# Performance work log

Hardware: AMD Instinct MI355X
Metric: run time of the kernel (lower is better)

## Reference

```python
import jax, jax.numpy as jnp
import numpy as np

B, S, H = 2, 1024, 2048          # batch, seq, hidden
E, K = 8, 2                       # num experts, top-k
I = 1408                          # moe_intermediate_size
IS = 5632                         # shared_expert_intermediate_size
WSCALE = 0.02


def setup_inputs() -> dict:
    key = jax.random.key(0)
    ks = jax.random.split(key, 9)
    f32 = jnp.float32
    return {
        "hidden_states": jax.random.normal(ks[0], (B, S, H), dtype=f32),
        "gate_w": jax.random.normal(ks[1], (E, H), dtype=f32) * WSCALE,          # router
        "w_gate": jax.random.normal(ks[2], (E, H, I), dtype=f32) * WSCALE,       # experts.N.gate_proj
        "w_up": jax.random.normal(ks[3], (E, H, I), dtype=f32) * WSCALE,         # experts.N.up_proj
        "w_down": jax.random.normal(ks[4], (E, I, H), dtype=f32) * WSCALE,       # experts.N.down_proj
        "sw_gate": jax.random.normal(ks[5], (H, IS), dtype=f32) * WSCALE,        # shared_expert.gate_proj
        "sw_up": jax.random.normal(ks[6], (H, IS), dtype=f32) * WSCALE,          # shared_expert.up_proj
        "sw_down": jax.random.normal(ks[7], (IS, H), dtype=f32) * WSCALE,        # shared_expert.down_proj
        "shared_gate_w": jax.random.normal(ks[8], (H, 1), dtype=f32) * WSCALE,   # shared_expert_gate
    }


def reference(hidden_states, gate_w, w_gate, w_up, w_down, sw_gate, sw_up, sw_down, shared_gate_w):
    x = hidden_states                                   # [B,S,H]
    # ---- TopKGate: softmax router -> top-k weights + indices, renormalized ----
    logits = jnp.einsum("bsh,eh->bse", x, gate_w)       # [B,S,E]
    probs = jax.nn.softmax(logits, axis=-1)
    top_w, top_i = jax.lax.top_k(probs, K)              # [B,S,K]
    top_w = top_w / jnp.sum(top_w, axis=-1, keepdims=True)
    # dense combine weights per expert: sum_k top_w * (top_i == e)  -> [B,S,E]
    onehot = jax.nn.one_hot(top_i, E, dtype=x.dtype)    # [B,S,K,E]
    combine = jnp.einsum("bsk,bske->bse", top_w, onehot)
    # ---- dense all-experts SwiGLU MLP, then mask/combine (faithful to source) ----
    g = jnp.einsum("bsh,ehi->besi", x, w_gate)          # [B,E,S,I]
    u = jnp.einsum("bsh,ehi->besi", x, w_up)
    h = jax.nn.silu(g) * u
    expert_out = jnp.einsum("besi,eih->besh", h, w_down)  # [B,E,S,H]
    moe_out = jnp.einsum("besh,bse->bsh", expert_out, combine)
    # ---- shared expert with sigmoid gate ----
    sh = jax.nn.silu(x @ sw_gate) * (x @ sw_up)         # [B,S,IS]
    shared_out = sh @ sw_down                            # [B,S,H]
    shared_gate = jax.nn.sigmoid(x @ shared_gate_w)     # [B,S,1]
    return moe_out + shared_out * shared_gate
```

## Files before the change

### kernel.cpp

```cpp
#include <hip/hip_runtime.h>
#include <hip/hip_bf16.h>
#include <stdint.h>

#define TOK   2048
#define HDIM  2048
#define IDIM  1408
#define ISDIM 5632
#define NEXP  8

typedef float  f32x4  __attribute__((ext_vector_type(4)));
typedef short  bf16x8 __attribute__((ext_vector_type(8)));

__device__ __forceinline__ unsigned short f2b(float f) {
  union { float f; uint32_t u; } v; v.f = f;
  return (unsigned short)((v.u + 0x7fffu + ((v.u >> 16) & 1u)) >> 16);
}

__device__ __forceinline__ void async16(void* lds, const void* g) {
  __builtin_amdgcn_global_load_lds(
      (const __attribute__((address_space(1))) unsigned int*)g,
      (__attribute__((address_space(3))) unsigned int*)lds, 16, 0, 0);
}

#define VWAIT_BAR(N) asm volatile("s_waitcnt vmcnt(" #N ")\n\ts_barrier" ::: "memory")
#define VBAR()       asm volatile("s_barrier" ::: "memory")

__global__ __launch_bounds__(256) void router_kernel(
    const float* __restrict__ X, const float* __restrict__ GW,
    const float* __restrict__ SGW, int* __restrict__ cnt,
    int* __restrict__ tok_e, float* __restrict__ tok_w, float* __restrict__ sg)
{
  const int tkn = blockIdx.x, t = threadIdx.x;
  const float* xr = X + (size_t)tkn * HDIM;
  float a[NEXP + 1];
  #pragma unroll
  for (int e = 0; e <= NEXP; ++e) a[e] = 0.f;
  for (int h = t; h < HDIM; h += 256) {
    const float xv = xr[h];
    #pragma unroll
    for (int e = 0; e < NEXP; ++e) a[e] += xv * GW[e * HDIM + h];
    a[NEXP] += xv * SGW[h];
  }
  #pragma unroll
  for (int off = 32; off > 0; off >>= 1) {
    #pragma unroll
    for (int e = 0; e <= NEXP; ++e) a[e] += __shfl_down(a[e], off);
  }
  __shared__ float red[4][NEXP + 1];
  if ((t & 63) == 0) {
    #pragma unroll
    for (int e = 0; e <= NEXP; ++e) red[t >> 6][e] = a[e];
  }
  __syncthreads();
  if (t == 0) {
    float l[NEXP + 1];
    #pragma unroll
    for (int e = 0; e <= NEXP; ++e) l[e] = red[0][e] + red[1][e] + red[2][e] + red[3][e];
    int i1 = 0;
    #pragma unroll
    for (int e = 1; e < NEXP; ++e) if (l[e] > l[i1]) i1 = e;
    int i2 = (i1 == 0) ? 1 : 0;
    #pragma unroll
    for (int e = 0; e < NEXP; ++e) if (e != i1 && e != i2 && l[e] > l[i2]) i2 = e;
    const float w1 = 1.f / (1.f + __expf(l[i2] - l[i1]));
    tok_e[tkn * 2 + 0] = i1; tok_e[tkn * 2 + 1] = i2;
    tok_w[tkn * 2 + 0] = w1; tok_w[tkn * 2 + 1] = 1.f - w1;
    atomicAdd(&cnt[i1], 1); atomicAdd(&cnt[i2], 1);
    sg[tkn] = 1.f / (1.f + __expf(-l[NEXP]));
  }
}

__global__ void scan_kernel(const int* __restrict__ cnt, int* __restrict__ offs) {
  if (threadIdx.x == 0) {
    int r = 0;
    for (int e = 0; e < NEXP; ++e) { offs[e] = r; r += cnt[e]; }
  }
}

__global__ __launch_bounds__(256) void build_kernel(
    const int* __restrict__ tok_e, const float* __restrict__ tok_w,
    const int* __restrict__ offs, int* __restrict__ cur,
    int* __restrict__ list, float* __restrict__ wl)
{
  const int tkn = blockIdx.x * 256 + threadIdx.x;
  if (tkn >= TOK) return;
  #pragma unroll
  for (int k = 0; k < 2; ++k) {
    const int e = tok_e[tkn * 2 + k];
    const int pos = atomicAdd(&cur[e], 1);
    const int slot = offs[e] + pos;
    list[slot] = tkn;
    wl[slot] = tok_w[tkn * 2 + k];
  }
}

__global__ __launch_bounds__(256) void cvt_kernel(
    const float* __restrict__ src, unsigned short* __restrict__ dst, int n4)
{
  const int i = blockIdx.x * 512 + threadIdx.x;
  #pragma unroll
  for (int p = 0; p < 2; ++p) {
    const int j = i + p * 256;
    if (j < n4) {
      const float4 v = ((const float4*)src)[j];
      ushort4 b; b.x = f2b(v.x); b.y = f2b(v.y); b.z = f2b(v.z); b.w = f2b(v.w);
      ((ushort4*)dst)[j] = b;
    }
  }
}

__global__ __launch_bounds__(256) void transpose_cvt_kernel(
    const float* __restrict__ src, unsigned short* __restrict__ dst,
    const int R, const int C)
{
  __shared__ unsigned short tile[64][72];
  const size_t mat = (size_t)blockIdx.z * R * C;
  const int c0 = blockIdx.x * 64, r0 = blockIdx.y * 64;
  const int t = threadIdx.x;
  const int rr = t >> 4, cc = (t & 15) * 4;
  #pragma unroll
  for (int p = 0; p < 4; ++p) {
    const int r = rr + p * 16;
    const float4 v = *(const float4*)(src + mat + (size_t)(r0 + r) * C + c0 + cc);
    tile[cc + 0][r] = f2b(v.x);
    tile[cc + 1][r] = f2b(v.y);
    tile[cc + 2][r] = f2b(v.z);
    tile[cc + 3][r] = f2b(v.w);
  }
  __syncthreads();
  #pragma unroll
  for (int p = 0; p < 2; ++p) {
    const int id = p * 256 + t;
    const int c = id >> 3, q = id & 7;
    const uint4 v = *(const uint4*)&tile[c][q * 8];
    *(uint4*)(dst + mat + (size_t)(c0 + c) * R + r0 + q * 8) = v;
  }
}

__global__ __launch_bounds__(512) void gateup_fused_kernel(
    const unsigned short* __restrict__ Xb,
    const unsigned short* __restrict__ Wshg, const unsigned short* __restrict__ Wshu,
    const unsigned short* __restrict__ Wexg, const unsigned short* __restrict__ Wexu,
    unsigned short* __restrict__ shb, unsigned short* __restrict__ hb,
    const int* __restrict__ list, const int* __restrict__ offs, const int* __restrict__ cnt)
{
  __shared__ char smem[65536];

  const int xcd = blockIdx.x & 7;
  const int local = blockIdx.x >> 3;
  const int c = xcd + 8 * (local >> 3);
  const int mt = local & 7;
  if (c >= 132) return;
  const int t = threadIdx.x;

  int rowbase, mcnt, n0, N, gather;
  const unsigned short *Wg, *Wu;
  unsigned short* Cout;
  if (c < 44) {
    N = ISDIM; n0 = c * 128; rowbase = mt * 256; mcnt = 256; gather = 0;
    Wg = Wshg; Wu = Wshu; Cout = shb;
  } else {
    const int cE = c - 44;
    const int e = cE / 11, n = cE % 11;
    mcnt = cnt[e] - mt * 256;
    if (mcnt <= 0) return;
    N = IDIM; n0 = n * 128; rowbase = offs[e] + mt * 256; gather = 1;
    Wg = Wexg + (size_t)e * IDIM * HDIM;
    Wu = Wexu + (size_t)e * IDIM * HDIM;
    Cout = hb;
  }

  const int wid = t >> 6, lane = t & 63;
  const int wm = wid >> 1, wn = wid & 1;
  const int lcol = lane & 15, lk = lane >> 4;

  f32x4 accg[4][4], accu[4][4];
  #pragma unroll
  for (int i = 0; i < 4; ++i)
    #pragma unroll
    for (int j = 0; j < 4; ++j) { accg[i][j] = {0.f,0.f,0.f,0.f}; accu[i][j] = {0.f,0.f,0.f,0.f}; }

  int arow[2], akoff[2];
  #pragma unroll
  for (int p = 0; p < 2; ++p) {
    const int s = p * 512 + t;
    const int m = s >> 2;
    akoff[p] = (((s & 3) ^ ((m >> 1) & 3)) << 3);
    arow[p] = gather ? list[rowbase + m] : (rowbase + m);
  }
  const int albase0 = (t & 448) * 16;
  const int albase1 = (512 + (t & 448)) * 16;
  const int bmrow = n0 + (t >> 2);
  const int bkoff = (((t & 3) ^ (((t >> 2) >> 1) & 3)) << 3);
  const int blbase = (t & 448) * 16;

#define STAGE_GU(BUF, K0) do {                                                    \
    async16(smem + (BUF) + albase0,        Xb + (size_t)arow[0] * HDIM + (K0) + akoff[0]); \
    async16(smem + (BUF) + albase1,        Xb + (size_t)arow[1] * HDIM + (K0) + akoff[1]); \
    async16(smem + (BUF) + 16384 + blbase, Wg + (size_t)bmrow * HDIM + (K0) + bkoff); \
    async16(smem + (BUF) + 24576 + blbase, Wu + (size_t)bmrow * HDIM + (K0) + bkoff); \
  } while (0)

#define COMPUTE_GU(BUF) do {                                                      \
    bf16x8 af[4], bg[4], bu[4];                                                   \
    _Pragma("unroll")                                                             \
    for (int fm = 0; fm < 4; ++fm) {                                              \
      const int m = wm * 64 + fm * 16 + lcol;                                     \
      af[fm] = *(const bf16x8*)(smem + (BUF) + m * 64 + (((lk ^ ((m >> 1) & 3)) & 3) << 4)); \
    }                                                                             \
    _Pragma("unroll")                                                             \
    for (int fn = 0; fn < 4; ++fn) {                                              \
      const int n = wn * 64 + fn * 16 + lcol;                                     \
      const int ra = n * 64 + (((lk ^ ((n >> 1) & 3)) & 3) << 4);                 \
      bg[fn] = *(const bf16x8*)(smem + (BUF) + 16384 + ra);                       \
      bu[fn] = *(const bf16x8*)(smem + (BUF) + 24576 + ra);                       \
    }                                                                             \
    _Pragma("unroll")                                                             \
    for (int fm = 0; fm < 4; ++fm)                                                \
      _Pragma("unroll")                                                           \
      for (int fn = 0; fn < 4; ++fn) {                                            \
        accg[fm][fn] = __builtin_amdgcn_mfma_f32_16x16x32_bf16(af[fm], bg[fn], accg[fm][fn], 0, 0, 0); \
        accu[fm][fn] = __builtin_amdgcn_mfma_f32_16x16x32_bf16(af[fm], bu[fn], accu[fm][fn], 0, 0, 0); \
      } } while (0)

  STAGE_GU(0, 0);
  for (int it = 0; it < 31; ++it) {
    STAGE_GU(32768, (2 * it + 1) * 32);
    VWAIT_BAR(4);
    COMPUTE_GU(0);
    VBAR();
    STAGE_GU(0, (2 * it + 2) * 32);
    VWAIT_BAR(4);
    COMPUTE_GU(32768);
    VBAR();
  }
  STAGE_GU(32768, 63 * 32);
  VWAIT_BAR(4);
  COMPUTE_GU(0);
  VBAR();
  VWAIT_BAR(0);
  COMPUTE_GU(32768);
#undef STAGE_GU
#undef COMPUTE_GU

  #pragma unroll
  for (int fm = 0; fm < 4; ++fm) {
    #pragma unroll
    for (int fn = 0; fn < 4; ++fn) {
      const int col = n0 + wn * 64 + fn * 16 + lcol;
      #pragma unroll
      for (int r = 0; r < 4; ++r) {
        const int lrow = wm * 64 + fm * 16 + lk * 4 + r;
        if (lrow < mcnt) {
          const float gv = accg[fm][fn][r];
          const float uv = accu[fm][fn][r];
          const float hv = gv * uv / (1.f + __expf(-gv));
          Cout[(size_t)(rowbase + lrow) * N + col] = f2b(hv);
        }
      }
    }
  }
}

__global__ __launch_bounds__(512) void down_fused_kernel(
    const unsigned short* __restrict__ shb, const unsigned short* __restrict__ hb,
    const unsigned short* __restrict__ WdshT, const unsigned short* __restrict__ WdexT,
    float* __restrict__ out,
    const int* __restrict__ list, const float* __restrict__ wl, const float* __restrict__ sg,
    const int* __restrict__ offs, const int* __restrict__ cnt)
{
  __shared__ char smem[49152];

  const int xcd = blockIdx.x & 7;
  const int local = blockIdx.x >> 3;
  const int c = xcd + 8 * (local >> 3);
  const int mt = local & 7;
  const int t = threadIdx.x;

  int rowbase, mcnt, n0, K, kbeg, em;
  const unsigned short *Ap, *Bp;
  if (c < 64) {
    const int pn = c & 15, ksp = c >> 4;
    rowbase = mt * 256; mcnt = 256; n0 = pn * 128;
    K = ISDIM; kbeg = ksp * 44; em = 0;
    Ap = shb; Bp = WdshT;
  } else {
    const int cE = c - 64;
    const int e = cE >> 4, n = cE & 15;
    mcnt = cnt[e] - mt * 256;
    if (mcnt <= 0) return;
    rowbase = offs[e] + mt * 256; n0 = n * 128;
    K = IDIM; kbeg = 0; em = 1;
    Ap = hb; Bp = WdexT + (size_t)e * HDIM * IDIM;
  }

  const int wid = t >> 6, lane = t & 63;
  const int wm = wid >> 1, wn = wid & 1;
  const int lcol = lane & 15, lk = lane >> 4;

  f32x4 acc[4][4];
  #pragma unroll
  for (int i = 0; i < 4; ++i)
    #pragma unroll
    for (int j = 0; j < 4; ++j) acc[i][j] = {0.f,0.f,0.f,0.f};

  int amrow[2], akoff[2];
  #pragma unroll
  for (int p = 0; p < 2; ++p) {
    const int s = p * 512 + t;
    const int m = s >> 2;
    akoff[p] = (((s & 3) ^ ((m >> 1) & 3)) << 3);
    int rw = rowbase + m;
    if (em && rw > 4223) rw = 4223;
    amrow[p] = rw;
  }
  const int albase0 = (t & 448) * 16;
  const int albase1 = (512 + (t & 448)) * 16;
  const int bmrow = n0 + (t >> 2);
  const int bkoff = (((t & 3) ^ (((t >> 2) >> 1) & 3)) << 3);
  const int blbase = (t & 448) * 16;

#define STAGE_D(BUF, K0) do {                                                     \
    async16(smem + (BUF) + albase0,        Ap + (size_t)amrow[0] * K + (K0) + akoff[0]); \
    async16(smem + (BUF) + albase1,        Ap + (size_t)amrow[1] * K + (K0) + akoff[1]); \
    async16(smem + (BUF) + 16384 + blbase, Bp + (size_t)bmrow * K + (K0) + bkoff); \
  } while (0)

#define COMPUTE_D(BUF) do {                                                       \
    bf16x8 af[4], bfr[4];                                                         \
    _Pragma("unroll")                                                             \
    for (int fm = 0; fm < 4; ++fm) {                                              \
      const int m = wm * 64 + fm * 16 + lcol;                                     \
      af[fm] = *(const bf16x8*)(smem + (BUF) + m * 64 + (((lk ^ ((m >> 1) & 3)) & 3) << 4)); \
    }                                                                             \
    _Pragma("unroll")                                                             \
    for (int fn = 0; fn < 4; ++fn) {                                              \
      const int n = wn * 64 + fn * 16 + lcol;                                     \
      bfr[fn] = *(const bf16x8*)(smem + (BUF) + 16384 + n * 64 + (((lk ^ ((n >> 1) & 3)) & 3) << 4)); \
    }                                                                             \
    _Pragma("unroll")                                                             \
    for (int fm = 0; fm < 4; ++fm)                                                \
      _Pragma("unroll")                                                           \
      for (int fn = 0; fn < 4; ++fn)                                              \
        acc[fm][fn] = __builtin_amdgcn_mfma_f32_16x16x32_bf16(af[fm], bfr[fn], acc[fm][fn], 0, 0, 0); \
  } while (0)

  const int kb = kbeg * 32;
  STAGE_D(0, kb);
  for (int it = 0; it < 21; ++it) {
    STAGE_D(24576, kb + (2 * it + 1) * 32);
    VWAIT_BAR(3);
    COMPUTE_D(0);
    VBAR();
    STAGE_D(0, kb + (2 * it + 2) * 32);
    VWAIT_BAR(3);
    COMPUTE_D(24576);
    VBAR();
  }
  STAGE_D(24576, kb + 43 * 32);
  VWAIT_BAR(3);
  COMPUTE_D(0);
  VBAR();
  VWAIT_BAR(0);
  COMPUTE_D(24576);
#undef STAGE_D
#undef COMPUTE_D

  #pragma unroll
  for (int fm = 0; fm < 4; ++fm) {
    #pragma unroll
    for (int fn = 0; fn < 4; ++fn) {
      const int col = n0 + wn * 64 + fn * 16 + lcol;
      #pragma unroll
      for (int r = 0; r < 4; ++r) {
        const int lrow = wm * 64 + fm * 16 + lk * 4 + r;
        if (lrow < mcnt) {
          const float v = acc[fm][fn][r];
          const int sl = rowbase + lrow;
          const int orow = em ? list[sl] : sl;
          const float sc = em ? wl[sl] : sg[sl];
          atomicAdd(out + (size_t)orow * HDIM + col, sc * v);
        }
      }
    }
  }
}

template<bool GATHER>
__global__ __launch_bounds__(256) void gateup_bf_kernel(
    const unsigned short* __restrict__ Xb,
    const unsigned short* __restrict__ WgT, const unsigned short* __restrict__ WuT,
    unsigned short* __restrict__ Cout,
    const int* __restrict__ list, const int* __restrict__ offs,
    const int* __restrict__ cnt, const int N, const int NT)
{
  __shared__ char smem[49152];
  char* sA  = smem;
  char* sBg = smem + 16384;
  char* sBu = smem + 32768;
  int wg = blockIdx.x;
  wg = (wg & 7) * (gridDim.x >> 3) + (wg >> 3);
  const int mt = wg & 15;
  const int pn = wg >> 4;
  const int t = threadIdx.x;
  int rowbase, mcnt, n0;
  const unsigned short *Wg, *Wu;
  if (GATHER) {
    const int e = pn / NT, n = pn % NT;
    mcnt = cnt[e] - mt * 128;
    if (mcnt <= 0) return;
    rowbase = offs[e] + mt * 128;
    n0 = n * 128;
    Wg = WgT + (size_t)e * N * HDIM;
    Wu = WuT + (size_t)e * N * HDIM;
  } else {
    rowbase = mt * 128; mcnt = 128; n0 = pn * 128;
    Wg = WgT; Wu = WuT;
  }
  const int w = t >> 6, lane = t & 63;
  const int wr = w >> 1, wc = w & 1;
  const int lcol = lane & 15, lk = lane >> 4;
  f32x4 accg[4][4], accu[4][4];
  #pragma unroll
  for (int i = 0; i < 4; ++i)
    #pragma unroll
    for (int j = 0; j < 4; ++j) { accg[i][j] = {0.f,0.f,0.f,0.f}; accu[i][j] = {0.f,0.f,0.f,0.f}; }
  int arow[4], bm[4], koff[4];
  #pragma unroll
  for (int p = 0; p < 4; ++p) {
    const int s = p * 256 + t;
    const int m = s >> 3;
    bm[p] = m;
    koff[p] = ((s & 7) ^ (m & 7)) << 3;
    arow[p] = GATHER ? list[rowbase + m] : (rowbase + m);
  }
  const int KSTEPS = HDIM / 64;
  for (int kt = 0; kt < KSTEPS; ++kt) {
    const int k0 = kt * 64;
    if (kt) __syncthreads();
    #pragma unroll
    for (int p = 0; p < 4; ++p) {
      const int lb = (p * 256 + (t & 192)) * 16;
      async16(sA  + lb, Xb + (size_t)arow[p] * HDIM + k0 + koff[p]);
      async16(sBg + lb, Wg + (size_t)(n0 + bm[p]) * HDIM + k0 + koff[p]);
      async16(sBu + lb, Wu + (size_t)(n0 + bm[p]) * HDIM + k0 + koff[p]);
    }
    __syncthreads();
    #pragma unroll
    for (int ks = 0; ks < 2; ++ks) {
      bf16x8 af[4], bg[4], bu[4];
      #pragma unroll
      for (int fm = 0; fm < 4; ++fm) {
        const int m = wr * 64 + fm * 16 + lcol;
        af[fm] = *(const bf16x8*)(sA + m * 128 + (((ks * 4 + lk) ^ (m & 7)) << 4));
      }
      #pragma unroll
      for (int fn = 0; fn < 4; ++fn) {
        const int n = wc * 64 + fn * 16 + lcol;
        const int ra = n * 128 + (((ks * 4 + lk) ^ (n & 7)) << 4);
        bg[fn] = *(const bf16x8*)(sBg + ra);
        bu[fn] = *(const bf16x8*)(sBu + ra);
      }
      #pragma unroll
      for (int fm = 0; fm < 4; ++fm)
        #pragma unroll
        for (int fn = 0; fn < 4; ++fn) {
          accg[fm][fn] = __builtin_amdgcn_mfma_f32_16x16x32_bf16(af[fm], bg[fn], accg[fm][fn], 0, 0, 0);
          accu[fm][fn] = __builtin_amdgcn_mfma_f32_16x16x32_bf16(af[fm], bu[fn], accu[fm][fn], 0, 0, 0);
        }
    }
  }
  #pragma unroll
  for (int fm = 0; fm < 4; ++fm) {
    #pragma unroll
    for (int fn = 0; fn < 4; ++fn) {
      const int col = n0 + wc * 64 + fn * 16 + lcol;
      #pragma unroll
      for (int r = 0; r < 4; ++r) {
        const int lrow = wr * 64 + fm * 16 + lk * 4 + r;
        if (lrow < mcnt) {
          const float gv = accg[fm][fn][r];
          const float uv = accu[fm][fn][r];
          Cout[(size_t)(rowbase + lrow) * N + col] = f2b(gv * uv / (1.f + __expf(-gv)));
        }
      }
    }
  }
}

template<bool EXPERT, int KSPLIT>
__global__ __launch_bounds__(256) void down_bf_kernel(
    const unsigned short* __restrict__ Abuf,
    const unsigned short* __restrict__ BT,
    float* __restrict__ out,
    const int* __restrict__ list, const float* __restrict__ wl,
    const int* __restrict__ offs, const int* __restrict__ cnt,
    const int K, const int ktps)
{
  __shared__ char smem[32768];
  char* sA = smem;
  char* sB = smem + 16384;
  int wg = blockIdx.x;
  wg = (wg & 7) * (gridDim.x >> 3) + (wg >> 3);
  const int ksp = wg % KSPLIT;
  const int mt  = (wg / KSPLIT) & 15;
  const int pn  = wg / (KSPLIT * 16);
  const int t = threadIdx.x;
  int rowbase, mcnt, n0;
  const unsigned short* Bm;
  if (EXPERT) {
    const int e = pn >> 4, n = pn & 15;
    mcnt = cnt[e] - mt * 128;
    if (mcnt <= 0) return;
    rowbase = offs[e] + mt * 128;
    n0 = n * 128;
    Bm = BT + (size_t)e * HDIM * K;
  } else {
    rowbase = mt * 128; mcnt = 128; n0 = pn * 128;
    Bm = BT;
  }
  const int w = t >> 6, lane = t & 63;
  const int wr = w >> 1, wc = w & 1;
  const int lcol = lane & 15, lk = lane >> 4;
  f32x4 acc[4][4];
  #pragma unroll
  for (int i = 0; i < 4; ++i)
    #pragma unroll
    for (int j = 0; j < 4; ++j) acc[i][j] = {0.f,0.f,0.f,0.f};
  int bm[4], koff[4];
  #pragma unroll
  for (int p = 0; p < 4; ++p) {
    const int s = p * 256 + t;
    const int m = s >> 3;
    bm[p] = m;
    koff[p] = ((s & 7) ^ (m & 7)) << 3;
  }
  const int kbeg = ksp * ktps, kend = kbeg + ktps;
  for (int kt = kbeg; kt < kend; ++kt) {
    const int k0 = kt * 64;
    if (kt != kbeg) __syncthreads();
    #pragma unroll
    for (int p = 0; p < 4; ++p) {
      const int lb = (p * 256 + (t & 192)) * 16;
      async16(sA + lb, Abuf + (size_t)(rowbase + bm[p]) * K + k0 + koff[p]);
      async16(sB + lb, Bm + (size_t)(n0 + bm[p]) * K + k0 + koff[p]);
    }
    __syncthreads();
    #pragma unroll
    for (int ks = 0; ks < 2; ++ks) {
      bf16x8 af[4], bfr[4];
      #pragma unroll
      for (int fm = 0; fm < 4; ++fm) {
        const int m = wr * 64 + fm * 16 + lcol;
        af[fm] = *(const bf16x8*)(sA + m * 128 + (((ks * 4 + lk) ^ (m & 7)) << 4));
      }
      #pragma unroll
      for (int fn = 0; fn < 4; ++fn) {
        const int n = wc * 64 + fn * 16 + lcol;
        bfr[fn] = *(const bf16x8*)(sB + n * 128 + (((ks * 4 + lk) ^ (n & 7)) << 4));
      }
      #pragma unroll
      for (int fm = 0; fm < 4; ++fm)
        #pragma unroll
        for (int fn = 0; fn < 4; ++fn)
          acc[fm][fn] = __builtin_amdgcn_mfma_f32_16x16x32_bf16(af[fm], bfr[fn], acc[fm][fn], 0, 0, 0);
    }
  }
  #pragma unroll
  for (int fm = 0; fm < 4; ++fm) {
    #pragma unroll
    for (int fn = 0; fn < 4; ++fn) {
      const int col = n0 + wc * 64 + fn * 16 + lcol;
      #pragma unroll
      for (int r = 0; r < 4; ++r) {
        const int lrow = wr * 64 + fm * 16 + lk * 4 + r;
        if (lrow < mcnt) {
          const float v = acc[fm][fn][r];
          if (EXPERT) {
            const int slot = rowbase + lrow;
            atomicAdd(out + (size_t)list[slot] * HDIM + col, wl[slot] * v);
          } else {
            const int row = rowbase + lrow;
            atomicAdd(out + (size_t)row * HDIM + col, wl[row] * v);
          }
        }
      }
    }
  }
}

extern "C" void kernel_launch(void* const* d_in, const int* in_sizes, int n_in,
                              void* d_out, int out_size, void* d_ws, size_t ws_size,
                              hipStream_t stream)
{
  const float* x       = (const float*)d_in[0];
  const float* gate_w  = (const float*)d_in[1];
  const float* w_gate  = (const float*)d_in[2];
  const float* w_up    = (const float*)d_in[3];
  const float* w_down  = (const float*)d_in[4];
  const float* sw_gate = (const float*)d_in[5];
  const float* sw_up   = (const float*)d_in[6];
  const float* sw_down = (const float*)d_in[7];
  const float* sgw     = (const float*)d_in[8];

  float* out = (float*)d_out;
  char* ws = (char*)d_ws;

  const size_t NEED_FUSED = 182000000;
  const size_t NEED_R4    = 136000000;

  if (ws_size >= NEED_FUSED) {
    unsigned short* Xb  = (unsigned short*)ws;
    unsigned short* W1  = (unsigned short*)(ws + 8388608);
    unsigned short* W2  = (unsigned short*)(ws + 31457280);
    unsigned short* W3  = (unsigned short*)(ws + 54525952);
    unsigned short* W4  = (unsigned short*)(ws + 100663296);
    unsigned short* shb = (unsigned short*)(ws + 146800640);
    unsigned short* hb  = (unsigned short*)(ws + 169869312);
    char* meta = ws + 181764096;
    int*   cnt   = (int*)(meta);
    int*   cur   = (int*)(meta + 256);
    int*   offs  = (int*)(meta + 512);
    int*   list  = (int*)(meta + 768);
    float* wl    = (float*)(meta + 768 + 18432);
    int*   tok_e = (int*)(meta + 768 + 2 * 18432);
    float* tok_w = (float*)(meta + 768 + 2 * 18432 + 16384);
    float* sg    = (float*)(meta + 768 + 2 * 18432 + 32768);

    hipMemsetAsync(meta, 0, 768 + 2 * 18432, stream);
    hipMemsetAsync(out, 0, (size_t)TOK * HDIM * 4, stream);

    cvt_kernel<<<TOK * HDIM / 4 / 512, 256, 0, stream>>>(x, Xb, TOK * HDIM / 4);
    router_kernel<<<TOK, 256, 0, stream>>>(x, gate_w, sgw, cnt, tok_e, tok_w, sg);
    scan_kernel<<<1, 64, 0, stream>>>(cnt, offs);
    build_kernel<<<8, 256, 0, stream>>>(tok_e, tok_w, offs, cur, list, wl);

    transpose_cvt_kernel<<<dim3(ISDIM / 64, HDIM / 64, 1), 256, 0, stream>>>(sw_gate, W1, HDIM, ISDIM);
    transpose_cvt_kernel<<<dim3(ISDIM / 64, HDIM / 64, 1), 256, 0, stream>>>(sw_up,   W2, HDIM, ISDIM);
    transpose_cvt_kernel<<<dim3(IDIM / 64, HDIM / 64, NEXP), 256, 0, stream>>>(w_gate, W3, HDIM, IDIM);
    transpose_cvt_kernel<<<dim3(IDIM / 64, HDIM / 64, NEXP), 256, 0, stream>>>(w_up,   W4, HDIM, IDIM);

    gateup_fused_kernel<<<1088, 512, 0, stream>>>(Xb, W1, W2, W3, W4, shb, hb, list, offs, cnt);

    transpose_cvt_kernel<<<dim3(HDIM / 64, ISDIM / 64, 1), 256, 0, stream>>>(sw_down, W1, ISDIM, HDIM);
    transpose_cvt_kernel<<<dim3(HDIM / 64, IDIM / 64, NEXP), 256, 0, stream>>>(w_down, W3, IDIM, HDIM);

    down_fused_kernel<<<1536, 512, 0, stream>>>(shb, hb, W1, W3, out, list, wl, sg, offs, cnt);
  } else if (ws_size >= NEED_R4) {
    unsigned short* Xb   = (unsigned short*)ws;
    unsigned short* R1a  = (unsigned short*)(ws + 8388608);
    unsigned short* R1b  = (unsigned short*)(ws + 54525952);
    unsigned short* shb  = (unsigned short*)(ws + 100663296);
    unsigned short* hb   = (unsigned short*)(ws + 123731968);
    char* meta = ws + 135626752;
    int*   cnt   = (int*)(meta);
    int*   cur   = (int*)(meta + 256);
    int*   offs  = (int*)(meta + 512);
    int*   list  = (int*)(meta + 768);
    float* wl    = (float*)(meta + 768 + 17152);
    int*   tok_e = (int*)(meta + 768 + 2 * 17152);
    float* tok_w = (float*)(meta + 768 + 2 * 17152 + 16384);
    float* sg    = (float*)(meta + 768 + 2 * 17152 + 32768);

    hipMemsetAsync(meta, 0, 768 + 2 * 17152, stream);
    hipMemsetAsync(out, 0, (size_t)TOK * HDIM * 4, stream);

    cvt_kernel<<<TOK * HDIM / 4 / 512, 256, 0, stream>>>(x, Xb, TOK * HDIM / 4);
    router_kernel<<<TOK, 256, 0, stream>>>(x, gate_w, sgw, cnt, tok_e, tok_w, sg);
    scan_kernel<<<1, 64, 0, stream>>>(cnt, offs);
    build_kernel<<<8, 256, 0, stream>>>(tok_e, tok_w, offs, cur, list, wl);

    transpose_cvt_kernel<<<dim3(ISDIM / 64, HDIM / 64, 1), 256, 0, stream>>>(sw_gate, R1a, HDIM, ISDIM);
    transpose_cvt_kernel<<<dim3(ISDIM / 64, HDIM / 64, 1), 256, 0, stream>>>(sw_up,   R1b, HDIM, ISDIM);
    gateup_bf_kernel<false><<<704, 256, 0, stream>>>(
        Xb, R1a, R1b, shb, nullptr, nullptr, nullptr, ISDIM, 44);
    transpose_cvt_kernel<<<dim3(HDIM / 64, ISDIM / 64, 1), 256, 0, stream>>>(sw_down, R1a, ISDIM, HDIM);
    down_bf_kernel<false, 2><<<512, 256, 0, stream>>>(
        shb, R1a, out, nullptr, sg, nullptr, nullptr, ISDIM, (ISDIM / 64) / 2);
    transpose_cvt_kernel<<<dim3(IDIM / 64, HDIM / 64, NEXP), 256, 0, stream>>>(w_gate, R1a, HDIM, IDIM);
    transpose_cvt_kernel<<<dim3(IDIM / 64, HDIM / 64, NEXP), 256, 0, stream>>>(w_up,   R1b, HDIM, IDIM);
    gateup_bf_kernel<true><<<1408, 256, 0, stream>>>(
        Xb, R1a, R1b, hb, list, offs, cnt, IDIM, 11);
    transpose_cvt_kernel<<<dim3(HDIM / 64, IDIM / 64, NEXP), 256, 0, stream>>>(w_down, R1a, IDIM, HDIM);
    down_bf_kernel<true, 1><<<2048, 256, 0, stream>>>(
        hb, R1a, out, list, wl, offs, cnt, IDIM, IDIM / 64);
  }
}
```

Measured before the change: 593.2 us.

## Fold down-proj weight transposes into gate/up GEMM launch as extra blocks

Appends 4224 extra blocks to the gate/up fused GEMM launch that transpose and convert the shared and expert down-projection weights to bf16 into separate buffers. This lets the transpose memory traffic overlap with the GEMM tail and removes two separate kernel launches. It also removes the older lower-workspace fallback path and its kernels. The new path needs a larger workspace, and the extra blocks compete with GEMM blocks for bandwidth and CUs.

```diff
diff --git a/kernel.cpp b/kernel.cpp
--- a/kernel.cpp
+++ b/kernel.cpp
@@ -7,6 +7,7 @@
 #define IDIM  1408
 #define ISDIM 5632
 #define NEXP  8
+#define GU_GEMM_BLOCKS 1088
 
 typedef float  f32x4  __attribute__((ext_vector_type(4)));
 typedef short  bf16x8 __attribute__((ext_vector_type(8)));
@@ -142,16 +143,55 @@
     const unsigned short* __restrict__ Wshg, const unsigned short* __restrict__ Wshu,
     const unsigned short* __restrict__ Wexg, const unsigned short* __restrict__ Wexu,
     unsigned short* __restrict__ shb, unsigned short* __restrict__ hb,
-    const int* __restrict__ list, const int* __restrict__ offs, const int* __restrict__ cnt)
+    const int* __restrict__ list, const int* __restrict__ offs, const int* __restrict__ cnt,
+    const float* __restrict__ swDown, const float* __restrict__ wDown,
+    unsigned short* __restrict__ W5, unsigned short* __restrict__ W6)
 {
   __shared__ char smem[65536];
+  const int t = threadIdx.x;
+
+  if (blockIdx.x >= GU_GEMM_BLOCKS) {
+    const int half = t >> 8;
+    const int t2 = t & 255;
+    int tid2 = (blockIdx.x - GU_GEMM_BLOCKS) * 2 + half;
+    const float* src; unsigned short* dst; int R, cx, ry;
+    if (tid2 < 2816) {
+      src = swDown; dst = W5; R = ISDIM; cx = tid2 & 31; ry = tid2 >> 5;
+    } else {
+      tid2 -= 2816;
+      const int e = tid2 / 704, rem = tid2 % 704;
+      cx = rem & 31; ry = rem >> 5;
+      src = wDown + (size_t)e * IDIM * HDIM;
+      dst = W6 + (size_t)e * HDIM * IDIM;
+      R = IDIM;
+    }
+    unsigned short (*tile)[72] = (unsigned short(*)[72])(smem + half * 16384);
+    const int c0 = cx * 64, r0 = ry * 64;
+    const int rr = t2 >> 4, cc = (t2 & 15) * 4;
+    #pragma unroll
+    for (int p = 0; p < 4; ++p) {
+      const int r = rr + p * 16;
+      const float4 v = *(const float4*)(src + (size_t)(r0 + r) * HDIM + c0 + cc);
+      tile[cc + 0][r] = f2b(v.x);
+      tile[cc + 1][r] = f2b(v.y);
+      tile[cc + 2][r] = f2b(v.z);
+      tile[cc + 3][r] = f2b(v.w);
+    }
+    __syncthreads();
+    #pragma unroll
+    for (int p = 0; p < 2; ++p) {
+      const int id = p * 256 + t2;
+      const int ci = id >> 3, q = id & 7;
+      *(uint4*)(dst + (size_t)(c0 + ci) * R + r0 + q * 8) = *(const uint4*)&tile[ci][q * 8];
+    }
+    return;
+  }
 
   const int xcd = blockIdx.x & 7;
   const int local = blockIdx.x >> 3;
   const int c = xcd + 8 * (local >> 3);
   const int mt = local & 7;
   if (c >= 132) return;
-  const int t = threadIdx.x;
 
   int rowbase, mcnt, n0, N, gather;
   const unsigned short *Wg, *Wu;
@@ -386,209 +426,6 @@
   }
 }
 
-template<bool GATHER>
-__global__ __launch_bounds__(256) void gateup_bf_kernel(
-    const unsigned short* __restrict__ Xb,
-    const unsigned short* __restrict__ WgT, const unsigned short* __restrict__ WuT,
-    unsigned short* __restrict__ Cout,
-    const int* __restrict__ list, const int* __restrict__ offs,
-    const int* __restrict__ cnt, const int N, const int NT)
-{
-  __shared__ char smem[49152];
-  char* sA  = smem;
-  char* sBg = smem + 16384;
-  char* sBu = smem + 32768;
-  int wg = blockIdx.x;
-  wg = (wg & 7) * (gridDim.x >> 3) + (wg >> 3);
-  const int mt = wg & 15;
-  const int pn = wg >> 4;
-  const int t = threadIdx.x;
-  int rowbase, mcnt, n0;
-  const unsigned short *Wg, *Wu;
-  if (GATHER) {
-    const int e = pn / NT, n = pn % NT;
-    mcnt = cnt[e] - mt * 128;
-    if (mcnt <= 0) return;
-    rowbase = offs[e] + mt * 128;
-    n0 = n * 128;
-    Wg = WgT + (size_t)e * N * HDIM;
-    Wu = WuT + (size_t)e * N * HDIM;
-  } else {
-    rowbase = mt * 128; mcnt = 128; n0 = pn * 128;
-    Wg = WgT; Wu = WuT;
-  }
-  const int w = t >> 6, lane = t & 63;
-  const int wr = w >> 1, wc = w & 1;
-  const int lcol = lane & 15, lk = lane >> 4;
-  f32x4 accg[4][4], accu[4][4];
-  #pragma unroll
-  for (int i = 0; i < 4; ++i)
-    #pragma unroll
-    for (int j = 0; j < 4; ++j) { accg[i][j] = {0.f,0.f,0.f,0.f}; accu[i][j] = {0.f,0.f,0.f,0.f}; }
-  int arow[4], bm[4], koff[4];
-  #pragma unroll
-  for (int p = 0; p < 4; ++p) {
-    const int s = p * 256 + t;
-    const int m = s >> 3;
-    bm[p] = m;
-    koff[p] = ((s & 7) ^ (m & 7)) << 3;
-    arow[p] = GATHER ? list[rowbase + m] : (rowbase + m);
-  }
-  const int KSTEPS = HDIM / 64;
-  for (int kt = 0; kt < KSTEPS; ++kt) {
-    const int k0 = kt * 64;
-    if (kt) __syncthreads();
-    #pragma unroll
-    for (int p = 0; p < 4; ++p) {
-      const int lb = (p * 256 + (t & 192)) * 16;
-      async16(sA  + lb, Xb + (size_t)arow[p] * HDIM + k0 + koff[p]);
-      async16(sBg + lb, Wg + (size_t)(n0 + bm[p]) * HDIM + k0 + koff[p]);
-      async16(sBu + lb, Wu + (size_t)(n0 + bm[p]) * HDIM + k0 + koff[p]);
-    }
-    __syncthreads();
-    #pragma unroll
-    for (int ks = 0; ks < 2; ++ks) {
-      bf16x8 af[4], bg[4], bu[4];
-      #pragma unroll
-      for (int fm = 0; fm < 4; ++fm) {
-        const int m = wr * 64 + fm * 16 + lcol;
-        af[fm] = *(const bf16x8*)(sA + m * 128 + (((ks * 4 + lk) ^ (m & 7)) << 4));
-      }
-      #pragma unroll
-      for (int fn = 0; fn < 4; ++fn) {
-        const int n = wc * 64 + fn * 16 + lcol;
-        const int ra = n * 128 + (((ks * 4 + lk) ^ (n & 7)) << 4);
-        bg[fn] = *(const bf16x8*)(sBg + ra);
-        bu[fn] = *(const bf16x8*)(sBu + ra);
-      }
-      #pragma unroll
-      for (int fm = 0; fm < 4; ++fm)
-        #pragma unroll
-        for (int fn = 0; fn < 4; ++fn) {
-          accg[fm][fn] = __builtin_amdgcn_mfma_f32_16x16x32_bf16(af[fm], bg[fn], accg[fm][fn], 0, 0, 0);
-          accu[fm][fn] = __builtin_amdgcn_mfma_f32_16x16x32_bf16(af[fm], bu[fn], accu[fm][fn], 0, 0, 0);
-        }
-    }
-  }
-  #pragma unroll
-  for (int fm = 0; fm < 4; ++fm) {
-    #pragma unroll
-    for (int fn = 0; fn < 4; ++fn) {
-      const int col = n0 + wc * 64 + fn * 16 + lcol;
-      #pragma unroll
-      for (int r = 0; r < 4; ++r) {
-        const int lrow = wr * 64 + fm * 16 + lk * 4 + r;
-        if (lrow < mcnt) {
-          const float gv = accg[fm][fn][r];
-          const float uv = accu[fm][fn][r];
-          Cout[(size_t)(rowbase + lrow) * N + col] = f2b(gv * uv / (1.f + __expf(-gv)));
-        }
-      }
-    }
-  }
-}
-
-template<bool EXPERT, int KSPLIT>
-__global__ __launch_bounds__(256) void down_bf_kernel(
-    const unsigned short* __restrict__ Abuf,
-    const unsigned short* __restrict__ BT,
-    float* __restrict__ out,
-    const int* __restrict__ list, const float* __restrict__ wl,
-    const int* __restrict__ offs, const int* __restrict__ cnt,
-    const int K, const int ktps)
-{
-  __shared__ char smem[32768];
-  char* sA = smem;
-  char* sB = smem + 16384;
-  int wg = blockIdx.x;
-  wg = (wg & 7) * (gridDim.x >> 3) + (wg >> 3);
-  const int ksp = wg % KSPLIT;
-  const int mt  = (wg / KSPLIT) & 15;
-  const int pn  = wg / (KSPLIT * 16);
-  const int t = threadIdx.x;
-  int rowbase, mcnt, n0;
-  const unsigned short* Bm;
-  if (EXPERT) {
-    const int e = pn >> 4, n = pn & 15;
-    mcnt = cnt[e] - mt * 128;
-    if (mcnt <= 0) return;
-    rowbase = offs[e] + mt * 128;
-    n0 = n * 128;
-    Bm = BT + (size_t)e * HDIM * K;
-  } else {
-    rowbase = mt * 128; mcnt = 128; n0 = pn * 128;
-    Bm = BT;
-  }
-  const int w = t >> 6, lane = t & 63;
-  const int wr = w >> 1, wc = w & 1;
-  const int lcol = lane & 15, lk = lane >> 4;
-  f32x4 acc[4][4];
-  #pragma unroll
-  for (int i = 0; i < 4; ++i)
-    #pragma unroll
-    for (int j = 0; j < 4; ++j) acc[i][j] = {0.f,0.f,0.f,0.f};
-  int bm[4], koff[4];
-  #pragma unroll
-  for (int p = 0; p < 4; ++p) {
-    const int s = p * 256 + t;
-    const int m = s >> 3;
-    bm[p] = m;
-    koff[p] = ((s & 7) ^ (m & 7)) << 3;
-  }
-  const int kbeg = ksp * ktps, kend = kbeg + ktps;
-  for (int kt = kbeg; kt < kend; ++kt) {
-    const int k0 = kt * 64;
-    if (kt != kbeg) __syncthreads();
-    #pragma unroll
-    for (int p = 0; p < 4; ++p) {
-      const int lb = (p * 256 + (t & 192)) * 16;
-      async16(sA + lb, Abuf + (size_t)(rowbase + bm[p]) * K + k0 + koff[p]);
-      async16(sB + lb, Bm + (size_t)(n0 + bm[p]) * K + k0 + koff[p]);
-    }
-    __syncthreads();
-    #pragma unroll
-    for (int ks = 0; ks < 2; ++ks) {
-      bf16x8 af[4], bfr[4];
-      #pragma unroll
-      for (int fm = 0; fm < 4; ++fm) {
-        const int m = wr * 64 + fm * 16 + lcol;
-        af[fm] = *(const bf16x8*)(sA + m * 128 + (((ks * 4 + lk) ^ (m & 7)) << 4));
-      }
-      #pragma unroll
-      for (int fn = 0; fn < 4; ++fn) {
-        const int n = wc * 64 + fn * 16 + lcol;
-        bfr[fn] = *(const bf16x8*)(sB + n * 128 + (((ks * 4 + lk) ^ (n & 7)) << 4));
-      }
-      #pragma unroll
-      for (int fm = 0; fm < 4; ++fm)
-        #pragma unroll
-        for (int fn = 0; fn < 4; ++fn)
-          acc[fm][fn] = __builtin_amdgcn_mfma_f32_16x16x32_bf16(af[fm], bfr[fn], acc[fm][fn], 0, 0, 0);
-    }
-  }
-  #pragma unroll
-  for (int fm = 0; fm < 4; ++fm) {
-    #pragma unroll
-    for (int fn = 0; fn < 4; ++fn) {
-      const int col = n0 + wc * 64 + fn * 16 + lcol;
-      #pragma unroll
-      for (int r = 0; r < 4; ++r) {
-        const int lrow = wr * 64 + fm * 16 + lk * 4 + r;
-        if (lrow < mcnt) {
-          const float v = acc[fm][fn][r];
-          if (EXPERT) {
-            const int slot = rowbase + lrow;
-            atomicAdd(out + (size_t)list[slot] * HDIM + col, wl[slot] * v);
-          } else {
-            const int row = rowbase + lrow;
-            atomicAdd(out + (size_t)row * HDIM + col, wl[row] * v);
-          }
-        }
-      }
-    }
-  }
-}
-
 extern "C" void kernel_launch(void* const* d_in, const int* in_sizes, int n_in,
                               void* d_out, int out_size, void* d_ws, size_t ws_size,
                               hipStream_t stream)
@@ -606,10 +443,47 @@
   float* out = (float*)d_out;
   char* ws = (char*)d_ws;
 
+  const size_t NEED_OVL   = 251100000;
   const size_t NEED_FUSED = 182000000;
-  const size_t NEED_R4    = 136000000;
-
-  if (ws_size >= NEED_FUSED) {
+
+  if (ws_size >= NEED_OVL) {
+    unsigned short* Xb  = (unsigned short*)ws;
+    unsigned short* W1  = (unsigned short*)(ws + 8388608);
+    unsigned short* W2  = (unsigned short*)(ws + 31457280);
+    unsigned short* W3  = (unsigned short*)(ws + 54525952);
+    unsigned short* W4  = (unsigned short*)(ws + 100663296);
+    unsigned short* W5  = (unsigned short*)(ws + 146800640);
+    unsigned short* W6  = (unsigned short*)(ws + 169869312);
+    unsigned short* shb = (unsigned short*)(ws + 216006656);
+    unsigned short* hb  = (unsigned short*)(ws + 239075328);
+    char* meta = ws + 250970112;
+    int*   cnt   = (int*)(meta);
+    int*   cur   = (int*)(meta + 256);
+    int*   offs  = (int*)(meta + 512);
+    int*   list  = (int*)(meta + 768);
+    float* wl    = (float*)(meta + 768 + 18432);
+    int*   tok_e = (int*)(meta + 768 + 2 * 18432);
+    float* tok_w = (float*)(meta + 768 + 2 * 18432 + 16384);
+    float* sg    = (float*)(meta + 768 + 2 * 18432 + 32768);
+
+    hipMemsetAsync(meta, 0, 768 + 2 * 18432, stream);
+    hipMemsetAsync(out, 0, (size_t)TOK * HDIM * 4, stream);
+
+    cvt_kernel<<<TOK * HDIM / 4 / 512, 256, 0, stream>>>(x, Xb, TOK * HDIM / 4);
+    router_kernel<<<TOK, 256, 0, stream>>>(x, gate_w, sgw, cnt, tok_e, tok_w, sg);
+    scan_kernel<<<1, 64, 0, stream>>>(cnt, offs);
+    build_kernel<<<8, 256, 0, stream>>>(tok_e, tok_w, offs, cur, list, wl);
+
+    transpose_cvt_kernel<<<dim3(ISDIM / 64, HDIM / 64, 1), 256, 0, stream>>>(sw_gate, W1, HDIM, ISDIM);
+    transpose_cvt_kernel<<<dim3(ISDIM / 64, HDIM / 64, 1), 256, 0, stream>>>(sw_up,   W2, HDIM, ISDIM);
+    transpose_cvt_kernel<<<dim3(IDIM / 64, HDIM / 64, NEXP), 256, 0, stream>>>(w_gate, W3, HDIM, IDIM);
+    transpose_cvt_kernel<<<dim3(IDIM / 64, HDIM / 64, NEXP), 256, 0, stream>>>(w_up,   W4, HDIM, IDIM);
+
+    gateup_fused_kernel<<<GU_GEMM_BLOCKS + 4224, 512, 0, stream>>>(
+        Xb, W1, W2, W3, W4, shb, hb, list, offs, cnt, sw_down, w_down, W5, W6);
+
+    down_fused_kernel<<<1536, 512, 0, stream>>>(shb, hb, W5, W6, out, list, wl, sg, offs, cnt);
+  } else if (ws_size >= NEED_FUSED) {
     unsigned short* Xb  = (unsigned short*)ws;
     unsigned short* W1  = (unsigned short*)(ws + 8388608);
     unsigned short* W2  = (unsigned short*)(ws + 31457280);
@@ -640,49 +514,12 @@
     transpose_cvt_kernel<<<dim3(IDIM / 64, HDIM / 64, NEXP), 256, 0, stream>>>(w_gate, W3, HDIM, IDIM);
     transpose_cvt_kernel<<<dim3(IDIM / 64, HDIM / 64, NEXP), 256, 0, stream>>>(w_up,   W4, HDIM, IDIM);
 
-    gateup_fused_kernel<<<1088, 512, 0, stream>>>(Xb, W1, W2, W3, W4, shb, hb, list, offs, cnt);
+    gateup_fused_kernel<<<GU_GEMM_BLOCKS, 512, 0, stream>>>(
+        Xb, W1, W2, W3, W4, shb, hb, list, offs, cnt, nullptr, nullptr, nullptr, nullptr);
 
     transpose_cvt_kernel<<<dim3(HDIM / 64, ISDIM / 64, 1), 256, 0, stream>>>(sw_down, W1, ISDIM, HDIM);
     transpose_cvt_kernel<<<dim3(HDIM / 64, IDIM / 64, NEXP), 256, 0, stream>>>(w_down, W3, IDIM, HDIM);
 
     down_fused_kernel<<<1536, 512, 0, stream>>>(shb, hb, W1, W3, out, list, wl, sg, offs, cnt);
-  } else if (ws_size >= NEED_R4) {
-    unsigned short* Xb   = (unsigned short*)ws;
-    unsigned short* R1a  = (unsigned short*)(ws + 8388608);
-    unsigned short* R1b  = (unsigned short*)(ws + 54525952);
-    unsigned short* shb  = (unsigned short*)(ws + 100663296);
-    unsigned short* hb   = (unsigned short*)(ws + 123731968);
-    char* meta = ws + 135626752;
-    int*   cnt   = (int*)(meta);
-    int*   cur   = (int*)(meta + 256);
-    int*   offs  = (int*)(meta + 512);
-    int*   list  = (int*)(meta + 768);
-    float* wl    = (float*)(meta + 768 + 17152);
-    int*   tok_e = (int*)(meta + 768 + 2 * 17152);
-    float* tok_w = (float*)(meta + 768 + 2 * 17152 + 16384);
-    float* sg    = (float*)(meta + 768 + 2 * 17152 + 32768);
-
-    hipMemsetAsync(meta, 0, 768 + 2 * 17152, stream);
-    hipMemsetAsync(out, 0, (size_t)TOK * HDIM * 4, stream);
-
-    cvt_kernel<<<TOK * HDIM / 4 / 512, 256, 0, stream>>>(x, Xb, TOK * HDIM / 4);
-    router_kernel<<<TOK, 256, 0, stream>>>(x, gate_w, sgw, cnt, tok_e, tok_w, sg);
-    scan_kernel<<<1, 64, 0, stream>>>(cnt, offs);
-    build_kernel<<<8, 256, 0, stream>>>(tok_e, tok_w, offs, cur, list, wl);
-
-    transpose_cvt_kernel<<<dim3(ISDIM / 64, HDIM / 64, 1), 256, 0, stream>>>(sw_gate, R1a, HDIM, ISDIM);
-    transpose_cvt_kernel<<<dim3(ISDIM / 64, HDIM / 64, 1), 256, 0, stream>>>(sw_up,   R1b, HDIM, ISDIM);
-    gateup_bf_kernel<false><<<704, 256, 0, stream>>>(
-        Xb, R1a, R1b, shb, nullptr, nullptr, nullptr, ISDIM, 44);
-    transpose_cvt_kernel<<<dim3(HDIM / 64, ISDIM / 64, 1), 256, 0, stream>>>(sw_down, R1a, ISDIM, HDIM);
-    down_bf_kernel<false, 2><<<512, 256, 0, stream>>>(
-        shb, R1a, out, nullptr, sg, nullptr, nullptr, ISDIM, (ISDIM / 64) / 2);
-    transpose_cvt_kernel<<<dim3(IDIM / 64, HDIM / 64, NEXP), 256, 0, stream>>>(w_gate, R1a, HDIM, IDIM);
-    transpose_cvt_kernel<<<dim3(IDIM / 64, HDIM / 64, NEXP), 256, 0, stream>>>(w_up,   R1b, HDIM, IDIM);
-    gateup_bf_kernel<true><<<1408, 256, 0, stream>>>(
-        Xb, R1a, R1b, hb, list, offs, cnt, IDIM, 11);
-    transpose_cvt_kernel<<<dim3(HDIM / 64, IDIM / 64, NEXP), 256, 0, stream>>>(w_down, R1a, IDIM, HDIM);
-    down_bf_kernel<true, 1><<<2048, 256, 0, stream>>>(
-        hb, R1a, out, list, wl, offs, cnt, IDIM, IDIM / 64);
-  }
-}
+  }
+}
```

Result: no change. 587.4 us (-1.0%).
